# Kernel tuning notes

Hardware: AMD Instinct MI355X
Metric: run time of the kernel (lower is better)

Reference implementation:

```python
import jax, jax.numpy as jnp
import numpy as np

D_MODEL, N_HEADS, D_FF = 1024, 16, 4096
NUM_FAMILIES, DICT_SIZE = 64, 16384
B, T = 2, 2048
EPS = 1e-6


def setup_inputs() -> dict:
    key = jax.random.key(0)
    ks = jax.random.split(key, 16)
    s = 0.02
    return {
        "x": jax.random.normal(ks[0], (B, T, D_MODEL), jnp.float32),
        "top_k": 8,
        "proto": jax.random.normal(ks[1], (NUM_FAMILIES, D_MODEL), jnp.float32) * s,
        "family_gate_w": jax.random.normal(ks[2], (NUM_FAMILIES, D_MODEL), jnp.float32) * s,
        "dict_w": jax.random.normal(ks[3], (DICT_SIZE, D_MODEL), jnp.float32) * s,
        "enc_w": jax.random.normal(ks[4], (DICT_SIZE, D_MODEL), jnp.float32) * s,
        "wq": jax.random.normal(ks[5], (D_MODEL, D_MODEL), jnp.float32) * s,
        "wk": jax.random.normal(ks[6], (D_MODEL, D_MODEL), jnp.float32) * s,
        "wv": jax.random.normal(ks[7], (D_MODEL, D_MODEL), jnp.float32) * s,
        "wo": jax.random.normal(ks[8], (D_MODEL, D_MODEL), jnp.float32) * s,
        "rel_templates": jax.random.normal(ks[9], (N_HEADS, D_MODEL // N_HEADS, D_MODEL // N_HEADS), jnp.float32) * s,
        "gate_proj_w": jax.random.normal(ks[10], (D_FF, D_MODEL), jnp.float32) * s,
        "up_proj_w": jax.random.normal(ks[11], (D_FF, D_MODEL), jnp.float32) * s,
        "down_proj_w": jax.random.normal(ks[12], (D_MODEL, D_FF), jnp.float32) * s,
        "norm1_w": jnp.ones((D_MODEL,), jnp.float32),
        "norm2_w": jnp.ones((D_MODEL,), jnp.float32),
        "bias_corr": jnp.zeros((D_MODEL,), jnp.float32),
    }


def _hc_norm(x, w):
    rms = jnp.sqrt(jnp.mean(x * x, axis=-1, keepdims=True) + EPS)
    return w * x / rms, jnp.mean(rms)


def _block(x, top_k, proto, family_gate_w, dict_w, enc_w, wq, wk, wv, wo,
           rel_templates, gate_proj_w, up_proj_w, down_proj_w,
           norm1_w, norm2_w, bias_corr):
    b, t, d = x.shape
    h = rel_templates.shape[0]
    dh = d // h
    m = dict_w.shape[0]

    # FamilyBasisPool
    family_scores = jax.nn.softmax(x @ family_gate_w.T, axis=-1)   # [b,t,K]
    basis = jnp.einsum('btk,kd->btd', family_scores, proto)

    # SparseOffsetDict on residual
    resid = x - basis
    coeffs = resid @ enc_w.T                                        # [b,t,M]
    topk_vals, topk_idx = jax.lax.top_k(coeffs, top_k)              # [b,t,k]
    # sparse scatter + einsum == gather rows of dictionary and weight them
    offset = jnp.einsum('btk,btkd->btd', topk_vals, dict_w[topk_idx])
    sparsity = jnp.sum(jnp.abs(topk_vals)) / (b * t * m)

    x_rec = basis + offset + bias_corr
    normed, e1 = _hc_norm(x_rec, norm1_w)

    # RelationProtocolLayer (k modulated by per-head templates)
    q = (normed @ wq.T).reshape(b, t, h, dh).transpose(0, 2, 1, 3)  # [b,h,t,dh]
    k = (normed @ wk.T).reshape(b, t, h, dh).transpose(0, 2, 1, 3)
    v = (normed @ wv.T).reshape(b, t, h, dh).transpose(0, 2, 1, 3)
    k_mod = jnp.einsum('bhtd,hde->bhte', k, rel_templates)
    attn = jax.nn.softmax(jnp.einsum('bhqd,bhkd->bhqk', q, k_mod) / jnp.sqrt(jnp.float32(dh)), axis=-1)
    out = jnp.einsum('bhqk,bhkd->bhqd', attn, v)
    out = out.transpose(0, 2, 1, 3).reshape(b, t, d) @ wo.T
    x = x + out

    normed2, e2 = _hc_norm(x, norm2_w)

    # ContextGatedRouter (sigmoid gate * silu up)
    gate = jax.nn.sigmoid(normed2 @ gate_proj_w.T)
    up = jax.nn.silu(normed2 @ up_proj_w.T)
    routed = (gate * up) @ down_proj_w.T
    x = x + routed
    return x, attn, family_scores, sparsity, e1, e2


def reference(x, top_k, proto, family_gate_w, dict_w, enc_w, wq, wk, wv, wo,
              rel_templates, gate_proj_w, up_proj_w, down_proj_w,
              norm1_w, norm2_w, bias_corr):
    return _block(x, top_k, proto, family_gate_w, dict_w, enc_w, wq, wk, wv, wo,
                  rel_templates, gate_proj_w, up_proj_w, down_proj_w,
                  norm1_w, norm2_w, bias_corr)
```

## Files before the change

kernel.cpp:

```cpp
#include <hip/hip_runtime.h>
#include <float.h>
#include <math.h>

#define D 1024
#define NF 64
#define MDICT 16384
#define NH 16
#define DH 64
#define TT 2048
#define ROWS 4096
#define DFF 4096

#define OUT_X     0LL
#define OUT_ATTN  4194304LL
#define OUT_FS    138412032LL
#define OUT_SPARS 138674176LL
#define OUT_E1    138674177LL
#define OUT_E2    138674178LL

typedef __attribute__((ext_vector_type(8))) short short8;
typedef __attribute__((ext_vector_type(4))) float f32x4;

__device__ inline unsigned short f2bf(float f) {
    unsigned int u = __float_as_uint(f);
    u = u + 0x7FFFu + ((u >> 16) & 1u);
    return (unsigned short)(u >> 16);
}
__device__ inline float bf2f(unsigned int s) {
    return __uint_as_float(s << 16);
}

__device__ inline float blk_sum(float v) {
    __shared__ float sb[4];
    int lane = threadIdx.x & 63, w = threadIdx.x >> 6;
#pragma unroll
    for (int o = 32; o; o >>= 1) v += __shfl_down(v, o);
    if (lane == 0) sb[w] = v;
    __syncthreads();
    float s = sb[0] + sb[1] + sb[2] + sb[3];
    __syncthreads();
    return s;
}

template<int BM, int BN, bool OBF, bool ACONV>
__global__ __launch_bounds__(256) void gemm_mfma(
    const void* __restrict__ Abv, const unsigned short* __restrict__ Bb,
    void* __restrict__ Cbv, const float* __restrict__ addCb,
    int K, int lda, int ldb, int ldc, float alpha, int batchH,
    long long aOut, long long aIn, long long bOut, long long bIn,
    long long cOut, long long cIn)
{
    int z = blockIdx.z;
    int zo = z / batchH, zi = z - zo * batchH;
    long long aoff = zo * aOut + zi * aIn;
    const unsigned short* B = Bb + zo * bOut + zi * bIn;
    long long cbase = zo * cOut + zi * cIn;
    const float* addC = addCb ? (addCb + cbase) : nullptr;

    __shared__ __align__(16) unsigned short As[BM * 32];
    __shared__ __align__(16) unsigned short Bs[BN * 32];

    int tid = threadIdx.x;
    int lane = tid & 63, wave = tid >> 6;
    int wr = wave >> 1, wc = wave & 1;
    long long r0 = (long long)blockIdx.y * BM;
    long long c0 = (long long)blockIdx.x * BN;

    constexpr int TI = BM / 32;
    constexpr int TJ = BN / 32;
    constexpr int RA = BM * 4 / 256;
    constexpr int RB = BN * 4 / 256;

    f32x4 acc[TI][TJ] = {};
    int lm = lane & 15;
    int kq = (lane >> 4) * 8;

    for (int k0 = 0; k0 < K; k0 += 32) {
        __syncthreads();
#pragma unroll
        for (int r = 0; r < RB; r++) {
            int q = r * 256 + tid;
            const unsigned short* gp = B + (c0 + (q >> 2)) * (long long)ldb + k0 + (q & 3) * 8;
            unsigned short* lp = Bs + (r * 256 + (tid & 192)) * 8;
            __builtin_amdgcn_global_load_lds(
                (const __attribute__((address_space(1))) void*)gp,
                (__attribute__((address_space(3))) void*)lp, 16, 0, 0);
        }
        if (ACONV) {
            const float* A = (const float*)Abv + aoff;
#pragma unroll
            for (int r = 0; r < RA; r++) {
                int q = r * 256 + tid;
                const float* gp = A + (r0 + (q >> 2)) * (long long)lda + k0 + (q & 3) * 8;
                float4 v0 = *(const float4*)gp;
                float4 v1 = *(const float4*)(gp + 4);
                short8 f;
                f[0] = (short)f2bf(v0.x); f[1] = (short)f2bf(v0.y);
                f[2] = (short)f2bf(v0.z); f[3] = (short)f2bf(v0.w);
                f[4] = (short)f2bf(v1.x); f[5] = (short)f2bf(v1.y);
                f[6] = (short)f2bf(v1.z); f[7] = (short)f2bf(v1.w);
                *(short8*)&As[q * 8] = f;
            }
        } else {
            const unsigned short* A = (const unsigned short*)Abv + aoff;
#pragma unroll
            for (int r = 0; r < RA; r++) {
                int q = r * 256 + tid;
                const unsigned short* gp = A + (r0 + (q >> 2)) * (long long)lda + k0 + (q & 3) * 8;
                unsigned short* lp = As + (r * 256 + (tid & 192)) * 8;
                __builtin_amdgcn_global_load_lds(
                    (const __attribute__((address_space(1))) void*)gp,
                    (__attribute__((address_space(3))) void*)lp, 16, 0, 0);
            }
        }
        __syncthreads();
        short8 af[TI], bfr[TJ];
#pragma unroll
        for (int i = 0; i < TI; i++)
            af[i] = *(const short8*)&As[(wr * (BM / 2) + i * 16 + lm) * 32 + kq];
#pragma unroll
        for (int j = 0; j < TJ; j++)
            bfr[j] = *(const short8*)&Bs[(wc * (BN / 2) + j * 16 + lm) * 32 + kq];
#pragma unroll
        for (int i = 0; i < TI; i++)
#pragma unroll
            for (int j = 0; j < TJ; j++)
                acc[i][j] = __builtin_amdgcn_mfma_f32_16x16x32_bf16(af[i], bfr[j], acc[i][j], 0, 0, 0);
    }

#pragma unroll
    for (int i = 0; i < TI; i++) {
#pragma unroll
        for (int r = 0; r < 4; r++) {
            long long row = r0 + wr * (BM / 2) + i * 16 + (lane >> 4) * 4 + r;
#pragma unroll
            for (int j = 0; j < TJ; j++) {
                long long col = c0 + wc * (BN / 2) + j * 16 + lm;
                long long idx = row * (long long)ldc + col;
                float v = alpha * acc[i][j][r];
                if (addC) v += addC[idx];
                if (OBF) ((unsigned short*)Cbv)[cbase + idx] = f2bf(v);
                else     ((float*)Cbv)[cbase + idx] = v;
            }
        }
    }
}

__global__ __launch_bounds__(256) void cvt_bf16_kernel(
    const float* __restrict__ in, unsigned short* __restrict__ out, long long n4)
{
    long long i = (long long)blockIdx.x * 256 + threadIdx.x;
    long long stride = (long long)gridDim.x * 256;
    for (; i < n4; i += stride) {
        float4 v = ((const float4*)in)[i];
        uint2 p;
        p.x = (unsigned)f2bf(v.x) | ((unsigned)f2bf(v.y) << 16);
        p.y = (unsigned)f2bf(v.z) | ((unsigned)f2bf(v.w) << 16);
        ((uint2*)out)[i] = p;
    }
}

__global__ __launch_bounds__(64) void family_kernel(
    const float* __restrict__ x, const float* __restrict__ fgw,
    float* __restrict__ fs_out)
{
    __shared__ float xs[D];
    int r = blockIdx.x, f = threadIdx.x;
    const float4* x4 = (const float4*)(x + (long long)r * D);
    float4* xs4 = (float4*)xs;
#pragma unroll
    for (int i = 0; i < 4; i++) xs4[f + 64 * i] = x4[f + 64 * i];
    __syncthreads();
    const float4* w4 = (const float4*)(fgw + (long long)f * D);
    float acc = 0.f;
#pragma unroll 8
    for (int d = 0; d < D / 4; d++) {
        float4 w = w4[d];
        float4 xv = xs4[d];
        acc += w.x * xv.x + w.y * xv.y + w.z * xv.z + w.w * xv.w;
    }
    float mx = acc;
#pragma unroll
    for (int o = 32; o; o >>= 1) mx = fmaxf(mx, __shfl_xor(mx, o));
    float e = __expf(acc - mx);
    float s = e;
#pragma unroll
    for (int o = 32; o; o >>= 1) s += __shfl_xor(s, o);
    fs_out[(long long)r * NF + f] = e / s;
}

__global__ __launch_bounds__(256) void basis_kernel(
    const float* __restrict__ x, const float* __restrict__ fs,
    const float* __restrict__ proto, float* __restrict__ basis,
    unsigned short* __restrict__ resid_bf)
{
    __shared__ float Ss[NF];
    int r = blockIdx.x, tid = threadIdx.x;
    if (tid < NF) Ss[tid] = fs[(long long)r * NF + tid];
    __syncthreads();
    float4 acc = {0.f, 0.f, 0.f, 0.f};
    const float4* p4 = (const float4*)proto;
#pragma unroll 8
    for (int k = 0; k < NF; k++) {
        float s = Ss[k];
        float4 p = p4[k * (D / 4) + tid];
        acc.x += s * p.x; acc.y += s * p.y; acc.z += s * p.z; acc.w += s * p.w;
    }
    long long base = (long long)r * (D / 4) + tid;
    float4 xv = ((const float4*)x)[base];
    ((float4*)basis)[base] = acc;
    uint2 rp;
    rp.x = (unsigned)f2bf(xv.x - acc.x) | ((unsigned)f2bf(xv.y - acc.y) << 16);
    rp.y = (unsigned)f2bf(xv.z - acc.z) | ((unsigned)f2bf(xv.w - acc.w) << 16);
    ((uint2*)resid_bf)[base] = rp;
}

__device__ inline void ins8(float v, int idx, float* vs, int* is) {
    if (v <= vs[7]) return;
    vs[7] = v; is[7] = idx;
#pragma unroll
    for (int j = 7; j > 0; j--) {
        if (vs[j] > vs[j - 1]) {
            float tv = vs[j]; vs[j] = vs[j - 1]; vs[j - 1] = tv;
            int ti = is[j]; is[j] = is[j - 1]; is[j - 1] = ti;
        }
    }
}

__global__ __launch_bounds__(256) void topk_kernel(
    const float* __restrict__ coeffs, float* __restrict__ tkv,
    int* __restrict__ tki, float* __restrict__ spars_acc)
{
    __shared__ float sv[2624];
    __shared__ int   si[2624];
    int r = blockIdx.x, tid = threadIdx.x;
    const float* row = coeffs + (long long)r * MDICT;
    float vs[8]; int is[8];
#pragma unroll
    for (int j = 0; j < 8; j++) { vs[j] = -FLT_MAX; is[j] = -1; }
    for (int s = 0; s < MDICT / 256; s++) {
        int col = s * 256 + tid;
        ins8(row[col], col, vs, is);
    }
#pragma unroll
    for (int j = 0; j < 8; j++) { sv[tid * 8 + j] = vs[j]; si[tid * 8 + j] = is[j]; }
    __syncthreads();
    if (tid < 64) {
#pragma unroll
        for (int j = 0; j < 8; j++) { vs[j] = -FLT_MAX; is[j] = -1; }
        for (int e = tid * 32; e < tid * 32 + 32; e++) ins8(sv[e], si[e], vs, is);
#pragma unroll
        for (int j = 0; j < 8; j++) { sv[2048 + tid * 8 + j] = vs[j]; si[2048 + tid * 8 + j] = is[j]; }
    }
    __syncthreads();
    if (tid < 8) {
#pragma unroll
        for (int j = 0; j < 8; j++) { vs[j] = -FLT_MAX; is[j] = -1; }
        for (int e = 2048 + tid * 64; e < 2048 + tid * 64 + 64; e++) ins8(sv[e], si[e], vs, is);
#pragma unroll
        for (int j = 0; j < 8; j++) { sv[2560 + tid * 8 + j] = vs[j]; si[2560 + tid * 8 + j] = is[j]; }
    }
    __syncthreads();
    if (tid == 0) {
#pragma unroll
        for (int j = 0; j < 8; j++) { vs[j] = -FLT_MAX; is[j] = -1; }
        for (int e = 2560; e < 2624; e++) ins8(sv[e], si[e], vs, is);
        float s = 0.f;
#pragma unroll
        for (int j = 0; j < 8; j++) {
            tkv[r * 8 + j] = vs[j];
            tki[r * 8 + j] = is[j];
            s += fabsf(vs[j]);
        }
        atomicAdd(spars_acc, s);
    }
}

__global__ __launch_bounds__(256) void xrec_norm_kernel(
    const float* __restrict__ basis, const float* __restrict__ dictw,
    const float* __restrict__ bias, const float* __restrict__ nw,
    const float* __restrict__ tkv, const int* __restrict__ tki,
    unsigned short* __restrict__ normed_bf, float* __restrict__ e_acc)
{
    int r = blockIdx.x, tid = threadIdx.x;
    float vals[8]; int idxs[8];
#pragma unroll
    for (int j = 0; j < 8; j++) { vals[j] = tkv[r * 8 + j]; idxs[j] = tki[r * 8 + j]; }
    long long base = (long long)r * (D / 4) + tid;
    float4 acc = ((const float4*)basis)[base];
    float4 bv = ((const float4*)bias)[tid];
    acc.x += bv.x; acc.y += bv.y; acc.z += bv.z; acc.w += bv.w;
#pragma unroll
    for (int j = 0; j < 8; j++) {
        float4 dv = ((const float4*)dictw)[(long long)idxs[j] * (D / 4) + tid];
        float v = vals[j];
        acc.x += v * dv.x; acc.y += v * dv.y; acc.z += v * dv.z; acc.w += v * dv.w;
    }
    float ss = acc.x * acc.x + acc.y * acc.y + acc.z * acc.z + acc.w * acc.w;
    float tot = blk_sum(ss);
    float rms = sqrtf(tot / (float)D + 1e-6f);
    if (tid == 0) atomicAdd(e_acc, rms);
    float inv = 1.f / rms;
    float4 wv = ((const float4*)nw)[tid];
    uint2 o;
    o.x = (unsigned)f2bf(acc.x * wv.x * inv) | ((unsigned)f2bf(acc.y * wv.y * inv) << 16);
    o.y = (unsigned)f2bf(acc.z * wv.z * inv) | ((unsigned)f2bf(acc.w * wv.w * inv) << 16);
    ((uint2*)normed_bf)[base] = o;
}

__global__ __launch_bounds__(256) void rmsnorm_kernel(
    const float* __restrict__ xin, const float* __restrict__ nw,
    unsigned short* __restrict__ xout_bf, float* __restrict__ e_acc)
{
    int r = blockIdx.x, tid = threadIdx.x;
    long long base = (long long)r * (D / 4) + tid;
    float4 v = ((const float4*)xin)[base];
    float ss = v.x * v.x + v.y * v.y + v.z * v.z + v.w * v.w;
    float tot = blk_sum(ss);
    float rms = sqrtf(tot / (float)D + 1e-6f);
    if (tid == 0) atomicAdd(e_acc, rms);
    float inv = 1.f / rms;
    float4 wv = ((const float4*)nw)[tid];
    uint2 o;
    o.x = (unsigned)f2bf(v.x * wv.x * inv) | ((unsigned)f2bf(v.y * wv.y * inv) << 16);
    o.y = (unsigned)f2bf(v.z * wv.z * inv) | ((unsigned)f2bf(v.w * wv.w * inv) << 16);
    ((uint2*)xout_bf)[base] = o;
}

__global__ __launch_bounds__(256) void kmod_kernel(
    const unsigned short* __restrict__ kb, const float* __restrict__ rel,
    unsigned short* __restrict__ kmod_bf)
{
    __shared__ float Rs[64 * 64];
    int z = blockIdx.y;
    int b = z >> 4, h = z & 15;
    int tid = threadIdx.x;
    const float4* r4 = (const float4*)(rel + (long long)h * 4096);
    float4* Rs4 = (float4*)Rs;
#pragma unroll
    for (int i = 0; i < 4; i++) Rs4[tid + 256 * i] = r4[tid + 256 * i];
    __syncthreads();
    int e = tid & 63, tl = tid >> 6;
    int t = blockIdx.x * 4 + tl;
    const unsigned short* krow = kb + ((long long)(b * TT + t)) * D + h * DH;
    float acc = 0.f;
#pragma unroll
    for (int d4 = 0; d4 < 16; d4++) {
        uint2 p = *(const uint2*)&krow[d4 * 4];
        acc += bf2f(p.x & 0xFFFFu) * Rs[(d4 * 4 + 0) * 64 + e];
        acc += bf2f(p.x >> 16)     * Rs[(d4 * 4 + 1) * 64 + e];
        acc += bf2f(p.y & 0xFFFFu) * Rs[(d4 * 4 + 2) * 64 + e];
        acc += bf2f(p.y >> 16)     * Rs[(d4 * 4 + 3) * 64 + e];
    }
    kmod_bf[(long long)z * (TT * DH) + t * 64 + e] = f2bf(acc);
}

__global__ __launch_bounds__(256) void vtrans_kernel(
    const unsigned short* __restrict__ vb, unsigned short* __restrict__ vT)
{
    __shared__ unsigned short tile[64][68];
    int z = blockIdx.y, b = z >> 4, h = z & 15;
    int t0 = blockIdx.x * 64;
    int tid = threadIdx.x;
    int tr = tid >> 4;
    int dc = (tid & 15) * 4;
#pragma unroll
    for (int r = 0; r < 4; r++) {
        int t = tr + r * 16;
        uint2 p = *(const uint2*)&vb[((long long)(b * TT + t0 + t)) * D + h * DH + dc];
        tile[t][dc] = (unsigned short)(p.x & 0xFFFFu);
        tile[t][dc + 1] = (unsigned short)(p.x >> 16);
        tile[t][dc + 2] = (unsigned short)(p.y & 0xFFFFu);
        tile[t][dc + 3] = (unsigned short)(p.y >> 16);
    }
    __syncthreads();
#pragma unroll
    for (int r = 0; r < 4; r++) {
        int d = tr + r * 16;
        int t = (tid & 15) * 4;
        uint2 p;
        p.x = (unsigned)tile[t][d] | ((unsigned)tile[t + 1][d] << 16);
        p.y = (unsigned)tile[t + 2][d] | ((unsigned)tile[t + 3][d] << 16);
        *(uint2*)&vT[(long long)z * 64 * TT + (long long)d * TT + t0 + t] = p;
    }
}

__global__ __launch_bounds__(256, 2) void attn_fused_kernel(
    const unsigned short* __restrict__ qb,
    const unsigned short* __restrict__ kmod,
    const unsigned short* __restrict__ vT,
    float* __restrict__ attn,
    unsigned short* __restrict__ ctx)
{
    constexpr int QS_LD = 72;
    constexpr int PS_LD = 136;
    __shared__ __align__(16) unsigned short Qs[128 * QS_LD];
    __shared__ __align__(16) unsigned short Ks[128 * QS_LD];
    __shared__ __align__(16) unsigned short Ps[128 * PS_LD];
    __shared__ float sm_h[2][128];
    __shared__ float sl_h[2][128];

    const int z = blockIdx.y;
    const int b = z >> 4, h = z & 15;
    const int q0 = blockIdx.x * 128;
    const int tid = threadIdx.x;
    const int lane = tid & 63;
    const int wave = tid >> 6;
    const int wr = wave >> 1, wc = wave & 1;
    const int lm = lane & 15, q4 = lane >> 4;
    const int kq = q4 * 8;

    {
        const unsigned short* qbase = qb + ((long long)(b * TT + q0)) * D + h * DH;
#pragma unroll
        for (int rr = 0; rr < 4; rr++) {
            int q = rr * 256 + tid;
            int row = q >> 3, seg = q & 7;
            short8 v = *(const short8*)(qbase + (long long)row * D + seg * 8);
            *(short8*)&Qs[row * QS_LD + seg * 8] = v;
        }
    }

    const unsigned short* kz = kmod + (long long)z * (TT * DH);

    float m_loc[4][4], l_loc[4][4];
#pragma unroll
    for (int i = 0; i < 4; i++)
#pragma unroll
        for (int r = 0; r < 4; r++) { m_loc[i][r] = -FLT_MAX; l_loc[i][r] = 0.f; }

    for (int kt = 0; kt < 16; kt++) {
        __syncthreads();
#pragma unroll
        for (int rr = 0; rr < 4; rr++) {
            int q = rr * 256 + tid;
            int row = q >> 3, seg = q & 7;
            short8 v = *(const short8*)(kz + (long long)(kt * 128 + row) * DH + seg * 8);
            *(short8*)&Ks[row * QS_LD + seg * 8] = v;
        }
        __syncthreads();
        f32x4 acc[4][4] = {};
#pragma unroll
        for (int ks = 0; ks < 2; ks++) {
            short8 af[4], bfk[4];
#pragma unroll
            for (int i = 0; i < 4; i++)
                af[i] = *(const short8*)&Qs[(wr * 64 + i * 16 + lm) * QS_LD + ks * 32 + kq];
#pragma unroll
            for (int j = 0; j < 4; j++)
                bfk[j] = *(const short8*)&Ks[(wc * 64 + j * 16 + lm) * QS_LD + ks * 32 + kq];
#pragma unroll
            for (int i = 0; i < 4; i++)
#pragma unroll
                for (int j = 0; j < 4; j++)
                    acc[i][j] = __builtin_amdgcn_mfma_f32_16x16x32_bf16(af[i], bfk[j], acc[i][j], 0, 0, 0);
        }
#pragma unroll
        for (int i = 0; i < 4; i++)
#pragma unroll
            for (int r = 0; r < 4; r++) {
                float v0 = acc[i][0][r] * 0.125f;
                float v1 = acc[i][1][r] * 0.125f;
                float v2 = acc[i][2][r] * 0.125f;
                float v3 = acc[i][3][r] * 0.125f;
                float tmax = fmaxf(fmaxf(v0, v1), fmaxf(v2, v3));
                float mo = m_loc[i][r];
                float mn = fmaxf(mo, tmax);
                l_loc[i][r] = l_loc[i][r] * __expf(mo - mn)
                            + __expf(v0 - mn) + __expf(v1 - mn)
                            + __expf(v2 - mn) + __expf(v3 - mn);
                m_loc[i][r] = mn;
            }
    }

#pragma unroll
    for (int off = 1; off <= 8; off <<= 1) {
#pragma unroll
        for (int i = 0; i < 4; i++)
#pragma unroll
            for (int r = 0; r < 4; r++) {
                float mo = __shfl_xor(m_loc[i][r], off);
                float lo = __shfl_xor(l_loc[i][r], off);
                float mn = fmaxf(m_loc[i][r], mo);
                l_loc[i][r] = l_loc[i][r] * __expf(m_loc[i][r] - mn) + lo * __expf(mo - mn);
                m_loc[i][r] = mn;
            }
    }
    if (lm == 0) {
#pragma unroll
        for (int i = 0; i < 4; i++)
#pragma unroll
            for (int r = 0; r < 4; r++) {
                int row = wr * 64 + i * 16 + q4 * 4 + r;
                sm_h[wc][row] = m_loc[i][r];
                sl_h[wc][row] = l_loc[i][r];
            }
    }
    __syncthreads();
    float Mf[4][4], Linv[4][4];
#pragma unroll
    for (int i = 0; i < 4; i++)
#pragma unroll
        for (int r = 0; r < 4; r++) {
            int row = wr * 64 + i * 16 + q4 * 4 + r;
            float m0 = sm_h[0][row], m1 = sm_h[1][row];
            float l0 = sl_h[0][row], l1 = sl_h[1][row];
            float mn = fmaxf(m0, m1);
            float L = l0 * __expf(m0 - mn) + l1 * __expf(m1 - mn);
            Mf[i][r] = mn;
            Linv[i][r] = 1.f / L;
        }

    const unsigned short* vz = vT + (long long)z * (64 * TT);
    float* az = attn + (long long)z * ((long long)TT * TT);
    f32x4 acc_o[4][2] = {};

    for (int kt = 0; kt < 16; kt++) {
        __syncthreads();
#pragma unroll
        for (int rr = 0; rr < 4; rr++) {
            int q = rr * 256 + tid;
            int row = q >> 3, seg = q & 7;
            short8 v = *(const short8*)(kz + (long long)(kt * 128 + row) * DH + seg * 8);
            *(short8*)&Ks[row * QS_LD + seg * 8] = v;
        }
        short8 bv[2][4];
#pragma unroll
        for (int j = 0; j < 2; j++)
#pragma unroll
            for (int ks = 0; ks < 4; ks++)
                bv[j][ks] = *(const short8*)(vz + (long long)(wc * 32 + j * 16 + lm) * TT
                                             + kt * 128 + ks * 32 + kq);
        __syncthreads();
        f32x4 acc[4][4] = {};
#pragma unroll
        for (int ks = 0; ks < 2; ks++) {
            short8 af[4], bfk[4];
#pragma unroll
            for (int i = 0; i < 4; i++)
                af[i] = *(const short8*)&Qs[(wr * 64 + i * 16 + lm) * QS_LD + ks * 32 + kq];
#pragma unroll
            for (int j = 0; j < 4; j++)
                bfk[j] = *(const short8*)&Ks[(wc * 64 + j * 16 + lm) * QS_LD + ks * 32 + kq];
#pragma unroll
            for (int i = 0; i < 4; i++)
#pragma unroll
                for (int j = 0; j < 4; j++)
                    acc[i][j] = __builtin_amdgcn_mfma_f32_16x16x32_bf16(af[i], bfk[j], acc[i][j], 0, 0, 0);
        }
#pragma unroll
        for (int i = 0; i < 4; i++)
#pragma unroll
            for (int r = 0; r < 4; r++) {
                int row = wr * 64 + i * 16 + q4 * 4 + r;
                float* arow = az + (long long)(q0 + row) * TT + kt * 128 + wc * 64 + lm;
#pragma unroll
                for (int j = 0; j < 4; j++) {
                    float p = __expf(acc[i][j][r] * 0.125f - Mf[i][r]) * Linv[i][r];
                    arow[j * 16] = p;
                    Ps[row * PS_LD + wc * 64 + j * 16 + lm] = f2bf(p);
                }
            }
        __syncthreads();
#pragma unroll
        for (int ks = 0; ks < 4; ks++) {
            short8 paf[4];
#pragma unroll
            for (int i = 0; i < 4; i++)
                paf[i] = *(const short8*)&Ps[(wr * 64 + i * 16 + lm) * PS_LD + ks * 32 + kq];
#pragma unroll
            for (int i = 0; i < 4; i++)
#pragma unroll
                for (int j = 0; j < 2; j++)
                    acc_o[i][j] = __builtin_amdgcn_mfma_f32_16x16x32_bf16(paf[i], bv[j][ks], acc_o[i][j], 0, 0, 0);
        }
    }

#pragma unroll
    for (int i = 0; i < 4; i++)
#pragma unroll
        for (int r = 0; r < 4; r++) {
            int row = wr * 64 + i * 16 + q4 * 4 + r;
            long long crow = ((long long)(b * TT + q0 + row)) * D + h * DH;
#pragma unroll
            for (int j = 0; j < 2; j++)
                ctx[crow + wc * 32 + j * 16 + lm] = f2bf(acc_o[i][j][r]);
        }
}

__global__ __launch_bounds__(256) void gateup_kernel(
    unsigned short* __restrict__ g, const unsigned short* __restrict__ u, long long n4)
{
    long long i = (long long)blockIdx.x * 256 + threadIdx.x;
    long long stride = (long long)gridDim.x * 256;
    for (; i < n4; i += stride) {
        uint2 gp = ((uint2*)g)[i];
        uint2 up = ((const uint2*)u)[i];
        float gv[4] = { bf2f(gp.x & 0xFFFFu), bf2f(gp.x >> 16), bf2f(gp.y & 0xFFFFu), bf2f(gp.y >> 16) };
        float uv[4] = { bf2f(up.x & 0xFFFFu), bf2f(up.x >> 16), bf2f(up.y & 0xFFFFu), bf2f(up.y >> 16) };
        unsigned short hh[4];
#pragma unroll
        for (int j = 0; j < 4; j++) {
            float r = (1.f / (1.f + __expf(-gv[j]))) * uv[j] * (1.f / (1.f + __expf(-uv[j])));
            hh[j] = f2bf(r);
        }
        uint2 o;
        o.x = (unsigned)hh[0] | ((unsigned)hh[1] << 16);
        o.y = (unsigned)hh[2] | ((unsigned)hh[3] << 16);
        ((uint2*)g)[i] = o;
    }
}

__global__ void finalize_kernel(const float* __restrict__ scal, float* __restrict__ out)
{
    out[OUT_SPARS] = scal[0] / (float)((double)ROWS * (double)MDICT);
    out[OUT_E1] = scal[1] / (float)ROWS;
    out[OUT_E2] = scal[2] / (float)ROWS;
}

extern "C" void kernel_launch(void* const* d_in, const int* in_sizes, int n_in,
                              void* d_out, int out_size, void* d_ws, size_t ws_size,
                              hipStream_t stream) {
    const float* x     = (const float*)d_in[0];
    const float* proto = (const float*)d_in[2];
    const float* fgw   = (const float*)d_in[3];
    const float* dictw = (const float*)d_in[4];
    const float* encw  = (const float*)d_in[5];
    const float* wq    = (const float*)d_in[6];
    const float* wk    = (const float*)d_in[7];
    const float* wv    = (const float*)d_in[8];
    const float* wo    = (const float*)d_in[9];
    const float* rel   = (const float*)d_in[10];
    const float* gatew = (const float*)d_in[11];
    const float* upw   = (const float*)d_in[12];
    const float* downw = (const float*)d_in[13];
    const float* n1w   = (const float*)d_in[14];
    const float* n2w   = (const float*)d_in[15];
    const float* bias  = (const float*)d_in[16];
    float* out = (float*)d_out;
    float* ws  = (float*)d_ws;

    float*          basisf  = ws + 0;
    unsigned short* kb_bf   = (unsigned short*)(ws + 4194304);
    unsigned short* resid_bf= (unsigned short*)(ws + 6291456);
    unsigned short* norm_bf = (unsigned short*)(ws + 8388608);
    unsigned short* qb_bf   = (unsigned short*)(ws + 10485760);
    unsigned short* vb_bf   = (unsigned short*)(ws + 12582912);
    unsigned short* kmod_bf = (unsigned short*)(ws + 14680064);
    unsigned short* vT_bf   = (unsigned short*)(ws + 16777216);
    unsigned short* encw_bf = (unsigned short*)(ws + 18874368);
    unsigned short* up_bf   = (unsigned short*)(ws + 27262976);
    unsigned short* wq_bf   = (unsigned short*)(ws + 35651584);
    unsigned short* wk_bf   = (unsigned short*)(ws + 36175872);
    unsigned short* wv_bf   = (unsigned short*)(ws + 36700160);
    unsigned short* wo_bf   = (unsigned short*)(ws + 37224448);
    unsigned short* gatew_bf= (unsigned short*)(ws + 37748736);
    unsigned short* upw_bf  = (unsigned short*)(ws + 39845888);
    unsigned short* downw_bf= (unsigned short*)(ws + 41943040);
    float*          tkv     = ws + 44040192;
    int*            tki     = (int*)(ws + 44072960);
    float*          scal    = ws + 44105728;
    unsigned short* ctx_bf  = resid_bf;
    unsigned short* gate_bf = encw_bf;
    float*          xmid    = basisf;

    float* fs   = out + OUT_FS;
    float* attn = out + OUT_ATTN;
    float* coeffs = attn;

    hipMemsetAsync(scal, 0, 3 * sizeof(float), stream);

    cvt_bf16_kernel<<<2048, 256, 0, stream>>>(encw, encw_bf, (long long)MDICT * D / 4);
    cvt_bf16_kernel<<<256, 256, 0, stream>>>(wq, wq_bf, (long long)D * D / 4);
    cvt_bf16_kernel<<<256, 256, 0, stream>>>(wk, wk_bf, (long long)D * D / 4);
    cvt_bf16_kernel<<<256, 256, 0, stream>>>(wv, wv_bf, (long long)D * D / 4);
    cvt_bf16_kernel<<<256, 256, 0, stream>>>(wo, wo_bf, (long long)D * D / 4);
    cvt_bf16_kernel<<<1024, 256, 0, stream>>>(gatew, gatew_bf, (long long)DFF * D / 4);
    cvt_bf16_kernel<<<1024, 256, 0, stream>>>(upw, upw_bf, (long long)DFF * D / 4);
    cvt_bf16_kernel<<<1024, 256, 0, stream>>>(downw, downw_bf, (long long)D * DFF / 4);

    family_kernel<<<ROWS, 64, 0, stream>>>(x, fgw, fs);
    basis_kernel<<<ROWS, 256, 0, stream>>>(x, fs, proto, basisf, resid_bf);
    gemm_mfma<128, 128, false, false><<<dim3(128, 32, 1), 256, 0, stream>>>(
        resid_bf, encw_bf, coeffs, nullptr, D, D, D, MDICT, 1.f, 1, 0, 0, 0, 0, 0, 0);
    topk_kernel<<<ROWS, 256, 0, stream>>>(coeffs, tkv, tki, scal + 0);
    xrec_norm_kernel<<<ROWS, 256, 0, stream>>>(basisf, dictw, bias, n1w, tkv, tki, norm_bf, scal + 1);
    gemm_mfma<128, 128, true, false><<<dim3(8, 32, 1), 256, 0, stream>>>(
        norm_bf, wq_bf, qb_bf, nullptr, D, D, D, D, 1.f, 1, 0, 0, 0, 0, 0, 0);
    gemm_mfma<128, 128, true, false><<<dim3(8, 32, 1), 256, 0, stream>>>(
        norm_bf, wk_bf, kb_bf, nullptr, D, D, D, D, 1.f, 1, 0, 0, 0, 0, 0, 0);
    gemm_mfma<128, 128, true, false><<<dim3(8, 32, 1), 256, 0, stream>>>(
        norm_bf, wv_bf, vb_bf, nullptr, D, D, D, D, 1.f, 1, 0, 0, 0, 0, 0, 0);
    kmod_kernel<<<dim3(TT / 4, 32), 256, 0, stream>>>(kb_bf, rel, kmod_bf);
    vtrans_kernel<<<dim3(TT / 64, 32), 256, 0, stream>>>(vb_bf, vT_bf);
    attn_fused_kernel<<<dim3(TT / 128, 32), 256, 0, stream>>>(
        qb_bf, kmod_bf, vT_bf, attn, ctx_bf);
    gemm_mfma<128, 128, false, false><<<dim3(8, 32, 1), 256, 0, stream>>>(
        ctx_bf, wo_bf, xmid, x, D, D, D, D, 1.f, 1, 0, 0, 0, 0, 0, 0);
    rmsnorm_kernel<<<ROWS, 256, 0, stream>>>(xmid, n2w, norm_bf, scal + 2);
    gemm_mfma<128, 128, true, false><<<dim3(32, 32, 1), 256, 0, stream>>>(
        norm_bf, gatew_bf, gate_bf, nullptr, D, D, D, DFF, 1.f, 1, 0, 0, 0, 0, 0, 0);
    gemm_mfma<128, 128, true, false><<<dim3(32, 32, 1), 256, 0, stream>>>(
        norm_bf, upw_bf, up_bf, nullptr, D, D, D, DFF, 1.f, 1, 0, 0, 0, 0, 0, 0);
    gateup_kernel<<<4096, 256, 0, stream>>>(gate_bf, up_bf, (long long)ROWS * DFF / 4);
    gemm_mfma<128, 128, false, false><<<dim3(8, 32, 1), 256, 0, stream>>>(
        gate_bf, downw_bf, out + OUT_X, xmid, DFF, DFF, DFF, D, 1.f, 1, 0, 0, 0, 0, 0, 0);
    finalize_kernel<<<1, 1, 0, stream>>>(scal, out);
}
```

Baseline: 2.026 ms.

## Fuse top-k into encoder GEMM, merge QKV and gate/up GEMMs, add XCD swizzle

The encoder GEMM now computes per-tile top-8 candidates in its epilogue, so the full 4096x16384 fp32 coefficient matrix is no longer written and re-read. A small reduction kernel then merges the candidates per row. The Q/K/V and gate/up projections are merged into single wider GEMMs that rely on the weight buffers being contiguous. Downstream kernels index into the interleaved outputs, and workgroups are swizzled across XCDs for cache locality. The fused epilogue adds shared-memory pressure and serial insertion work to the GEMM.

```diff
diff --git a/kernel.cpp b/kernel.cpp
--- a/kernel.cpp
+++ b/kernel.cpp
@@ -10,6 +10,7 @@
 #define TT 2048
 #define ROWS 4096
 #define DFF 4096
+#define QKV_LD 3072
 
 #define OUT_X     0LL
 #define OUT_ATTN  4194304LL
@@ -30,6 +31,12 @@
     return __uint_as_float(s << 16);
 }
 
+__device__ inline int xcd_swz(int wg, int nwg) {
+    int q = nwg >> 3, r = nwg & 7;
+    int xcd = wg & 7, loc = wg >> 3;
+    return (xcd < r ? xcd * (q + 1) : r * (q + 1) + (xcd - r) * q) + loc;
+}
+
 __device__ inline float blk_sum(float v) {
     __shared__ float sb[4];
     int lane = threadIdx.x & 63, w = threadIdx.x >> 6;
@@ -42,20 +49,19 @@
     return s;
 }
 
-template<int BM, int BN, bool OBF, bool ACONV>
+template<int BM, int BN, bool OBF>
 __global__ __launch_bounds__(256) void gemm_mfma(
-    const void* __restrict__ Abv, const unsigned short* __restrict__ Bb,
+    const unsigned short* __restrict__ Ab, const unsigned short* __restrict__ Bb,
     void* __restrict__ Cbv, const float* __restrict__ addCb,
-    int K, int lda, int ldb, int ldc, float alpha, int batchH,
-    long long aOut, long long aIn, long long bOut, long long bIn,
-    long long cOut, long long cIn)
-{
-    int z = blockIdx.z;
-    int zo = z / batchH, zi = z - zo * batchH;
-    long long aoff = zo * aOut + zi * aIn;
-    const unsigned short* B = Bb + zo * bOut + zi * bIn;
-    long long cbase = zo * cOut + zi * cIn;
-    const float* addC = addCb ? (addCb + cbase) : nullptr;
+    int K, int lda, int ldb, int ldc, float alpha)
+{
+    int nwg = gridDim.x * gridDim.y;
+    int wg = blockIdx.y * gridDim.x + blockIdx.x;
+    int swz = xcd_swz(wg, nwg);
+    int bx = swz % (int)gridDim.x, by = swz / (int)gridDim.x;
+
+    const unsigned short* B = Bb;
+    const float* addC = addCb;
 
     __shared__ __align__(16) unsigned short As[BM * 32];
     __shared__ __align__(16) unsigned short Bs[BN * 32];
@@ -63,8 +69,8 @@
     int tid = threadIdx.x;
     int lane = tid & 63, wave = tid >> 6;
     int wr = wave >> 1, wc = wave & 1;
-    long long r0 = (long long)blockIdx.y * BM;
-    long long c0 = (long long)blockIdx.x * BN;
+    long long r0 = (long long)by * BM;
+    long long c0 = (long long)bx * BN;
 
     constexpr int TI = BM / 32;
     constexpr int TJ = BN / 32;
@@ -86,32 +92,14 @@
                 (const __attribute__((address_space(1))) void*)gp,
                 (__attribute__((address_space(3))) void*)lp, 16, 0, 0);
         }
-        if (ACONV) {
-            const float* A = (const float*)Abv + aoff;
-#pragma unroll
-            for (int r = 0; r < RA; r++) {
-                int q = r * 256 + tid;
-                const float* gp = A + (r0 + (q >> 2)) * (long long)lda + k0 + (q & 3) * 8;
-                float4 v0 = *(const float4*)gp;
-                float4 v1 = *(const float4*)(gp + 4);
-                short8 f;
-                f[0] = (short)f2bf(v0.x); f[1] = (short)f2bf(v0.y);
-                f[2] = (short)f2bf(v0.z); f[3] = (short)f2bf(v0.w);
-                f[4] = (short)f2bf(v1.x); f[5] = (short)f2bf(v1.y);
-                f[6] = (short)f2bf(v1.z); f[7] = (short)f2bf(v1.w);
-                *(short8*)&As[q * 8] = f;
-            }
-        } else {
-            const unsigned short* A = (const unsigned short*)Abv + aoff;
-#pragma unroll
-            for (int r = 0; r < RA; r++) {
-                int q = r * 256 + tid;
-                const unsigned short* gp = A + (r0 + (q >> 2)) * (long long)lda + k0 + (q & 3) * 8;
-                unsigned short* lp = As + (r * 256 + (tid & 192)) * 8;
-                __builtin_amdgcn_global_load_lds(
-                    (const __attribute__((address_space(1))) void*)gp,
-                    (__attribute__((address_space(3))) void*)lp, 16, 0, 0);
-            }
+#pragma unroll
+        for (int r = 0; r < RA; r++) {
+            int q = r * 256 + tid;
+            const unsigned short* gp = Ab + (r0 + (q >> 2)) * (long long)lda + k0 + (q & 3) * 8;
+            unsigned short* lp = As + (r * 256 + (tid & 192)) * 8;
+            __builtin_amdgcn_global_load_lds(
+                (const __attribute__((address_space(1))) void*)gp,
+                (__attribute__((address_space(3))) void*)lp, 16, 0, 0);
         }
         __syncthreads();
         short8 af[TI], bfr[TJ];
@@ -139,10 +127,170 @@
                 long long idx = row * (long long)ldc + col;
                 float v = alpha * acc[i][j][r];
                 if (addC) v += addC[idx];
-                if (OBF) ((unsigned short*)Cbv)[cbase + idx] = f2bf(v);
-                else     ((float*)Cbv)[cbase + idx] = v;
+                if (OBF) ((unsigned short*)Cbv)[idx] = f2bf(v);
+                else     ((float*)Cbv)[idx] = v;
             }
         }
+    }
+}
+
+__device__ inline void ins8(float v, int idx, float* vs, int* is) {
+    if (v <= vs[7]) return;
+    vs[7] = v; is[7] = idx;
+#pragma unroll
+    for (int j = 7; j > 0; j--) {
+        if (vs[j] > vs[j - 1]) {
+            float tv = vs[j]; vs[j] = vs[j - 1]; vs[j - 1] = tv;
+            int ti = is[j]; is[j] = is[j - 1]; is[j - 1] = ti;
+        }
+    }
+}
+
+__global__ __launch_bounds__(256) void gemm_topk(
+    const unsigned short* __restrict__ Ab, const unsigned short* __restrict__ Bb,
+    float* __restrict__ cand_v, int* __restrict__ cand_i)
+{
+    constexpr int BM = 128, BN = 128;
+    constexpr int NBX = MDICT / BN;
+    int nwg = gridDim.x * gridDim.y;
+    int wg = blockIdx.y * gridDim.x + blockIdx.x;
+    int swz = xcd_swz(wg, nwg);
+    int bx = swz % (int)gridDim.x, by = swz / (int)gridDim.x;
+
+    __shared__ __align__(16) unsigned short As[BM * 32];
+    __shared__ __align__(16) unsigned short Bs[BN * 32];
+    __shared__ float Sv[64 * 133];
+
+    int tid = threadIdx.x;
+    int lane = tid & 63, wave = tid >> 6;
+    int wr = wave >> 1, wc = wave & 1;
+    long long r0 = (long long)by * BM;
+    long long c0 = (long long)bx * BN;
+
+    f32x4 acc[4][4] = {};
+    int lm = lane & 15;
+    int q4 = lane >> 4;
+    int kq = q4 * 8;
+
+    for (int k0 = 0; k0 < D; k0 += 32) {
+        __syncthreads();
+#pragma unroll
+        for (int r = 0; r < 2; r++) {
+            int q = r * 256 + tid;
+            const unsigned short* gp = Bb + (c0 + (q >> 2)) * (long long)D + k0 + (q & 3) * 8;
+            unsigned short* lp = Bs + (r * 256 + (tid & 192)) * 8;
+            __builtin_amdgcn_global_load_lds(
+                (const __attribute__((address_space(1))) void*)gp,
+                (__attribute__((address_space(3))) void*)lp, 16, 0, 0);
+        }
+#pragma unroll
+        for (int r = 0; r < 2; r++) {
+            int q = r * 256 + tid;
+            const unsigned short* gp = Ab + (r0 + (q >> 2)) * (long long)D + k0 + (q & 3) * 8;
+            unsigned short* lp = As + (r * 256 + (tid & 192)) * 8;
+            __builtin_amdgcn_global_load_lds(
+                (const __attribute__((address_space(1))) void*)gp,
+                (__attribute__((address_space(3))) void*)lp, 16, 0, 0);
+        }
+        __syncthreads();
+        short8 af[4], bfr[4];
+#pragma unroll
+        for (int i = 0; i < 4; i++)
+            af[i] = *(const short8*)&As[(wr * 64 + i * 16 + lm) * 32 + kq];
+#pragma unroll
+        for (int j = 0; j < 4; j++)
+            bfr[j] = *(const short8*)&Bs[(wc * 64 + j * 16 + lm) * 32 + kq];
+#pragma unroll
+        for (int i = 0; i < 4; i++)
+#pragma unroll
+            for (int j = 0; j < 4; j++)
+                acc[i][j] = __builtin_amdgcn_mfma_f32_16x16x32_bf16(af[i], bfr[j], acc[i][j], 0, 0, 0);
+    }
+
+#pragma unroll
+    for (int h = 0; h < 2; h++) {
+        __syncthreads();
+        if (wr == h) {
+#pragma unroll
+            for (int i = 0; i < 4; i++)
+#pragma unroll
+                for (int r = 0; r < 4; r++)
+#pragma unroll
+                    for (int j = 0; j < 4; j++)
+                        Sv[(i * 16 + q4 * 4 + r) * 133 + wc * 64 + j * 16 + lm] = acc[i][j][r];
+        }
+        __syncthreads();
+        int row_loc = tid >> 2, sub = tid & 3;
+        float vs[8]; int is[8];
+#pragma unroll
+        for (int k = 0; k < 8; k++) { vs[k] = -FLT_MAX; is[k] = -1; }
+        const float* Srow = &Sv[row_loc * 133 + sub * 32];
+        int cbase = (int)c0 + sub * 32;
+        for (int c = 0; c < 32; c++) ins8(Srow[c], cbase + c, vs, is);
+#pragma unroll
+        for (int step = 1; step <= 2; step <<= 1) {
+            float ov[8]; int oi[8];
+#pragma unroll
+            for (int k = 0; k < 8; k++) { ov[k] = __shfl_xor(vs[k], step); oi[k] = __shfl_xor(is[k], step); }
+#pragma unroll
+            for (int k = 0; k < 8; k++) ins8(ov[k], oi[k], vs, is);
+        }
+        if (sub == 0) {
+            long long grow = r0 + h * 64 + row_loc;
+#pragma unroll
+            for (int k = 0; k < 8; k++) {
+                cand_v[grow * (NBX * 8) + bx * 8 + k] = vs[k];
+                cand_i[grow * (NBX * 8) + bx * 8 + k] = is[k];
+            }
+        }
+    }
+}
+
+__global__ __launch_bounds__(256) void topk_reduce_kernel(
+    const float* __restrict__ cand_v, const int* __restrict__ cand_i,
+    float* __restrict__ tkv, int* __restrict__ tki, float* __restrict__ spars_acc)
+{
+    __shared__ float sv[2624];
+    __shared__ int   si[2624];
+    int r = blockIdx.x, tid = threadIdx.x;
+    float4 cv = ((const float4*)(cand_v + (long long)r * 1024))[tid];
+    int4   ci = ((const int4*)(cand_i + (long long)r * 1024))[tid];
+    float vs[8]; int is[8];
+#pragma unroll
+    for (int j = 0; j < 8; j++) { vs[j] = -FLT_MAX; is[j] = -1; }
+    ins8(cv.x, ci.x, vs, is); ins8(cv.y, ci.y, vs, is);
+    ins8(cv.z, ci.z, vs, is); ins8(cv.w, ci.w, vs, is);
+#pragma unroll
+    for (int j = 0; j < 8; j++) { sv[tid * 8 + j] = vs[j]; si[tid * 8 + j] = is[j]; }
+    __syncthreads();
+    if (tid < 64) {
+#pragma unroll
+        for (int j = 0; j < 8; j++) { vs[j] = -FLT_MAX; is[j] = -1; }
+        for (int e = tid * 32; e < tid * 32 + 32; e++) ins8(sv[e], si[e], vs, is);
+#pragma unroll
+        for (int j = 0; j < 8; j++) { sv[2048 + tid * 8 + j] = vs[j]; si[2048 + tid * 8 + j] = is[j]; }
+    }
+    __syncthreads();
+    if (tid < 8) {
+#pragma unroll
+        for (int j = 0; j < 8; j++) { vs[j] = -FLT_MAX; is[j] = -1; }
+        for (int e = 2048 + tid * 64; e < 2048 + tid * 64 + 64; e++) ins8(sv[e], si[e], vs, is);
+#pragma unroll
+        for (int j = 0; j < 8; j++) { sv[2560 + tid * 8 + j] = vs[j]; si[2560 + tid * 8 + j] = is[j]; }
+    }
+    __syncthreads();
+    if (tid == 0) {
+#pragma unroll
+        for (int j = 0; j < 8; j++) { vs[j] = -FLT_MAX; is[j] = -1; }
+        for (int e = 2560; e < 2624; e++) ins8(sv[e], si[e], vs, is);
+        float s = 0.f;
+#pragma unroll
+        for (int j = 0; j < 8; j++) {
+            tkv[r * 8 + j] = vs[j];
+            tki[r * 8 + j] = is[j];
+            s += fabsf(vs[j]);
+        }
+        atomicAdd(spars_acc, s);
     }
 }
 
@@ -213,67 +361,6 @@
     rp.x = (unsigned)f2bf(xv.x - acc.x) | ((unsigned)f2bf(xv.y - acc.y) << 16);
     rp.y = (unsigned)f2bf(xv.z - acc.z) | ((unsigned)f2bf(xv.w - acc.w) << 16);
     ((uint2*)resid_bf)[base] = rp;
-}
-
-__device__ inline void ins8(float v, int idx, float* vs, int* is) {
-    if (v <= vs[7]) return;
-    vs[7] = v; is[7] = idx;
-#pragma unroll
-    for (int j = 7; j > 0; j--) {
-        if (vs[j] > vs[j - 1]) {
-            float tv = vs[j]; vs[j] = vs[j - 1]; vs[j - 1] = tv;
-            int ti = is[j]; is[j] = is[j - 1]; is[j - 1] = ti;
-        }
-    }
-}
-
-__global__ __launch_bounds__(256) void topk_kernel(
-    const float* __restrict__ coeffs, float* __restrict__ tkv,
-    int* __restrict__ tki, float* __restrict__ spars_acc)
-{
-    __shared__ float sv[2624];
-    __shared__ int   si[2624];
-    int r = blockIdx.x, tid = threadIdx.x;
-    const float* row = coeffs + (long long)r * MDICT;
-    float vs[8]; int is[8];
-#pragma unroll
-    for (int j = 0; j < 8; j++) { vs[j] = -FLT_MAX; is[j] = -1; }
-    for (int s = 0; s < MDICT / 256; s++) {
-        int col = s * 256 + tid;
-        ins8(row[col], col, vs, is);
-    }
-#pragma unroll
-    for (int j = 0; j < 8; j++) { sv[tid * 8 + j] = vs[j]; si[tid * 8 + j] = is[j]; }
-    __syncthreads();
-    if (tid < 64) {
-#pragma unroll
-        for (int j = 0; j < 8; j++) { vs[j] = -FLT_MAX; is[j] = -1; }
-        for (int e = tid * 32; e < tid * 32 + 32; e++) ins8(sv[e], si[e], vs, is);
-#pragma unroll
-        for (int j = 0; j < 8; j++) { sv[2048 + tid * 8 + j] = vs[j]; si[2048 + tid * 8 + j] = is[j]; }
-    }
-    __syncthreads();
-    if (tid < 8) {
-#pragma unroll
-        for (int j = 0; j < 8; j++) { vs[j] = -FLT_MAX; is[j] = -1; }
-        for (int e = 2048 + tid * 64; e < 2048 + tid * 64 + 64; e++) ins8(sv[e], si[e], vs, is);
-#pragma unroll
-        for (int j = 0; j < 8; j++) { sv[2560 + tid * 8 + j] = vs[j]; si[2560 + tid * 8 + j] = is[j]; }
-    }
-    __syncthreads();
-    if (tid == 0) {
-#pragma unroll
-        for (int j = 0; j < 8; j++) { vs[j] = -FLT_MAX; is[j] = -1; }
-        for (int e = 2560; e < 2624; e++) ins8(sv[e], si[e], vs, is);
-        float s = 0.f;
-#pragma unroll
-        for (int j = 0; j < 8; j++) {
-            tkv[r * 8 + j] = vs[j];
-            tki[r * 8 + j] = is[j];
-            s += fabsf(vs[j]);
-        }
-        atomicAdd(spars_acc, s);
-    }
 }
 
 __global__ __launch_bounds__(256) void xrec_norm_kernel(
@@ -328,7 +415,7 @@
 }
 
 __global__ __launch_bounds__(256) void kmod_kernel(
-    const unsigned short* __restrict__ kb, const float* __restrict__ rel,
+    const unsigned short* __restrict__ qkv, const float* __restrict__ rel,
     unsigned short* __restrict__ kmod_bf)
 {
     __shared__ float Rs[64 * 64];
@@ -342,7 +429,7 @@
     __syncthreads();
     int e = tid & 63, tl = tid >> 6;
     int t = blockIdx.x * 4 + tl;
-    const unsigned short* krow = kb + ((long long)(b * TT + t)) * D + h * DH;
+    const unsigned short* krow = qkv + ((long long)(b * TT + t)) * QKV_LD + D + h * DH;
     float acc = 0.f;
 #pragma unroll
     for (int d4 = 0; d4 < 16; d4++) {
@@ -356,7 +443,7 @@
 }
 
 __global__ __launch_bounds__(256) void vtrans_kernel(
-    const unsigned short* __restrict__ vb, unsigned short* __restrict__ vT)
+    const unsigned short* __restrict__ qkv, unsigned short* __restrict__ vT)
 {
     __shared__ unsigned short tile[64][68];
     int z = blockIdx.y, b = z >> 4, h = z & 15;
@@ -367,7 +454,7 @@
 #pragma unroll
     for (int r = 0; r < 4; r++) {
         int t = tr + r * 16;
-        uint2 p = *(const uint2*)&vb[((long long)(b * TT + t0 + t)) * D + h * DH + dc];
+        uint2 p = *(const uint2*)&qkv[((long long)(b * TT + t0 + t)) * QKV_LD + 2 * D + h * DH + dc];
         tile[t][dc] = (unsigned short)(p.x & 0xFFFFu);
         tile[t][dc + 1] = (unsigned short)(p.x >> 16);
         tile[t][dc + 2] = (unsigned short)(p.y & 0xFFFFu);
@@ -386,7 +473,7 @@
 }
 
 __global__ __launch_bounds__(256, 2) void attn_fused_kernel(
-    const unsigned short* __restrict__ qb,
+    const unsigned short* __restrict__ qkv,
     const unsigned short* __restrict__ kmod,
     const unsigned short* __restrict__ vT,
     float* __restrict__ attn,
@@ -400,9 +487,12 @@
     __shared__ float sm_h[2][128];
     __shared__ float sl_h[2][128];
 
-    const int z = blockIdx.y;
+    int nwg = gridDim.x * gridDim.y;
+    int wg = blockIdx.y * gridDim.x + blockIdx.x;
+    int swz = xcd_swz(wg, nwg);
+    const int z = swz / (int)gridDim.x;
+    const int q0 = (swz % (int)gridDim.x) * 128;
     const int b = z >> 4, h = z & 15;
-    const int q0 = blockIdx.x * 128;
     const int tid = threadIdx.x;
     const int lane = tid & 63;
     const int wave = tid >> 6;
@@ -411,12 +501,12 @@
     const int kq = q4 * 8;
 
     {
-        const unsigned short* qbase = qb + ((long long)(b * TT + q0)) * D + h * DH;
+        const unsigned short* qbase = qkv + ((long long)(b * TT + q0)) * QKV_LD + h * DH;
 #pragma unroll
         for (int rr = 0; rr < 4; rr++) {
             int q = rr * 256 + tid;
             int row = q >> 3, seg = q & 7;
-            short8 v = *(const short8*)(qbase + (long long)row * D + seg * 8);
+            short8 v = *(const short8*)(qbase + (long long)row * QKV_LD + seg * 8);
             *(short8*)&Qs[row * QS_LD + seg * 8] = v;
         }
     }
@@ -589,15 +679,19 @@
 }
 
 __global__ __launch_bounds__(256) void gateup_kernel(
-    unsigned short* __restrict__ g, const unsigned short* __restrict__ u, long long n4)
+    unsigned short* __restrict__ gu, long long n4)
 {
     long long i = (long long)blockIdx.x * 256 + threadIdx.x;
     long long stride = (long long)gridDim.x * 256;
+    uint2* gu2 = (uint2*)gu;
     for (; i < n4; i += stride) {
-        uint2 gp = ((uint2*)g)[i];
-        uint2 up = ((const uint2*)u)[i];
-        float gv[4] = { bf2f(gp.x & 0xFFFFu), bf2f(gp.x >> 16), bf2f(gp.y & 0xFFFFu), bf2f(gp.y >> 16) };
-        float uv[4] = { bf2f(up.x & 0xFFFFu), bf2f(up.x >> 16), bf2f(up.y & 0xFFFFu), bf2f(up.y >> 16) };
+        long long row = i >> 10, c = i & 1023;
+        uint2* gp = gu2 + row * 2048 + c;
+        const uint2* up = gu2 + row * 2048 + 1024 + c;
+        uint2 g = *gp;
+        uint2 u = *up;
+        float gv[4] = { bf2f(g.x & 0xFFFFu), bf2f(g.x >> 16), bf2f(g.y & 0xFFFFu), bf2f(g.y >> 16) };
+        float uv[4] = { bf2f(u.x & 0xFFFFu), bf2f(u.x >> 16), bf2f(u.y & 0xFFFFu), bf2f(u.y >> 16) };
         unsigned short hh[4];
 #pragma unroll
         for (int j = 0; j < 4; j++) {
@@ -607,7 +701,7 @@
         uint2 o;
         o.x = (unsigned)hh[0] | ((unsigned)hh[1] << 16);
         o.y = (unsigned)hh[2] | ((unsigned)hh[3] << 16);
-        ((uint2*)g)[i] = o;
+        *gp = o;
     }
 }
 
@@ -641,15 +735,13 @@
     float* ws  = (float*)d_ws;
 
     float*          basisf  = ws + 0;
-    unsigned short* kb_bf   = (unsigned short*)(ws + 4194304);
-    unsigned short* resid_bf= (unsigned short*)(ws + 6291456);
-    unsigned short* norm_bf = (unsigned short*)(ws + 8388608);
-    unsigned short* qb_bf   = (unsigned short*)(ws + 10485760);
-    unsigned short* vb_bf   = (unsigned short*)(ws + 12582912);
-    unsigned short* kmod_bf = (unsigned short*)(ws + 14680064);
-    unsigned short* vT_bf   = (unsigned short*)(ws + 16777216);
+    unsigned short* qkv_bf  = (unsigned short*)(ws + 4194304);
+    unsigned short* kmod_bf = (unsigned short*)(ws + 10485760);
+    unsigned short* vT_bf   = (unsigned short*)(ws + 12582912);
+    unsigned short* resid_bf= (unsigned short*)(ws + 14680064);
+    unsigned short* norm_bf = (unsigned short*)(ws + 16777216);
     unsigned short* encw_bf = (unsigned short*)(ws + 18874368);
-    unsigned short* up_bf   = (unsigned short*)(ws + 27262976);
+    unsigned short* gu_bf   = (unsigned short*)(ws + 18874368);
     unsigned short* wq_bf   = (unsigned short*)(ws + 35651584);
     unsigned short* wk_bf   = (unsigned short*)(ws + 36175872);
     unsigned short* wv_bf   = (unsigned short*)(ws + 36700160);
@@ -661,12 +753,12 @@
     int*            tki     = (int*)(ws + 44072960);
     float*          scal    = ws + 44105728;
     unsigned short* ctx_bf  = resid_bf;
-    unsigned short* gate_bf = encw_bf;
     float*          xmid    = basisf;
 
     float* fs   = out + OUT_FS;
     float* attn = out + OUT_ATTN;
-    float* coeffs = attn;
+    float* cand_v = attn;
+    int*   cand_i = (int*)(attn + 4194304);
 
     hipMemsetAsync(scal, 0, 3 * sizeof(float), stream);
 
@@ -681,29 +773,22 @@
 
     family_kernel<<<ROWS, 64, 0, stream>>>(x, fgw, fs);
     basis_kernel<<<ROWS, 256, 0, stream>>>(x, fs, proto, basisf, resid_bf);
-    gemm_mfma<128, 128, false, false><<<dim3(128, 32, 1), 256, 0, stream>>>(
-        resid_bf, encw_bf, coeffs, nullptr, D, D, D, MDICT, 1.f, 1, 0, 0, 0, 0, 0, 0);
-    topk_kernel<<<ROWS, 256, 0, stream>>>(coeffs, tkv, tki, scal + 0);
+    gemm_topk<<<dim3(128, 32, 1), 256, 0, stream>>>(resid_bf, encw_bf, cand_v, cand_i);
+    topk_reduce_kernel<<<ROWS, 256, 0, stream>>>(cand_v, cand_i, tkv, tki, scal + 0);
     xrec_norm_kernel<<<ROWS, 256, 0, stream>>>(basisf, dictw, bias, n1w, tkv, tki, norm_bf, scal + 1);
-    gemm_mfma<128, 128, true, false><<<dim3(8, 32, 1), 256, 0, stream>>>(
-        norm_bf, wq_bf, qb_bf, nullptr, D, D, D, D, 1.f, 1, 0, 0, 0, 0, 0, 0);
-    gemm_mfma<128, 128, true, false><<<dim3(8, 32, 1), 256, 0, stream>>>(
-        norm_bf, wk_bf, kb_bf, nullptr, D, D, D, D, 1.f, 1, 0, 0, 0, 0, 0, 0);
-    gemm_mfma<128, 128, true, false><<<dim3(8, 32, 1), 256, 0, stream>>>(
-        norm_bf, wv_bf, vb_bf, nullptr, D, D, D, D, 1.f, 1, 0, 0, 0, 0, 0, 0);
-    kmod_kernel<<<dim3(TT / 4, 32), 256, 0, stream>>>(kb_bf, rel, kmod_bf);
-    vtrans_kernel<<<dim3(TT / 64, 32), 256, 0, stream>>>(vb_bf, vT_bf);
+    gemm_mfma<128, 128, true><<<dim3(24, 32, 1), 256, 0, stream>>>(
+        norm_bf, wq_bf, qkv_bf, nullptr, D, D, D, QKV_LD, 1.f);
+    kmod_kernel<<<dim3(TT / 4, 32), 256, 0, stream>>>(qkv_bf, rel, kmod_bf);
+    vtrans_kernel<<<dim3(TT / 64, 32), 256, 0, stream>>>(qkv_bf, vT_bf);
     attn_fused_kernel<<<dim3(TT / 128, 32), 256, 0, stream>>>(
-        qb_bf, kmod_bf, vT_bf, attn, ctx_bf);
-    gemm_mfma<128, 128, false, false><<<dim3(8, 32, 1), 256, 0, stream>>>(
-        ctx_bf, wo_bf, xmid, x, D, D, D, D, 1.f, 1, 0, 0, 0, 0, 0, 0);
+        qkv_bf, kmod_bf, vT_bf, attn, ctx_bf);
+    gemm_mfma<128, 128, false><<<dim3(8, 32, 1), 256, 0, stream>>>(
+        ctx_bf, wo_bf, xmid, x, D, D, D, D, 1.f);
     rmsnorm_kernel<<<ROWS, 256, 0, stream>>>(xmid, n2w, norm_bf, scal + 2);
-    gemm_mfma<128, 128, true, false><<<dim3(32, 32, 1), 256, 0, stream>>>(
-        norm_bf, gatew_bf, gate_bf, nullptr, D, D, D, DFF, 1.f, 1, 0, 0, 0, 0, 0, 0);
-    gemm_mfma<128, 128, true, false><<<dim3(32, 32, 1), 256, 0, stream>>>(
-        norm_bf, upw_bf, up_bf, nullptr, D, D, D, DFF, 1.f, 1, 0, 0, 0, 0, 0, 0);
-    gateup_kernel<<<4096, 256, 0, stream>>>(gate_bf, up_bf, (long long)ROWS * DFF / 4);
-    gemm_mfma<128, 128, false, false><<<dim3(8, 32, 1), 256, 0, stream>>>(
-        gate_bf, downw_bf, out + OUT_X, xmid, DFF, DFF, DFF, D, 1.f, 1, 0, 0, 0, 0, 0, 0);
+    gemm_mfma<128, 128, true><<<dim3(64, 32, 1), 256, 0, stream>>>(
+        norm_bf, gatew_bf, gu_bf, nullptr, D, D, D, 2 * DFF, 1.f);
+    gateup_kernel<<<4096, 256, 0, stream>>>(gu_bf, (long long)ROWS * DFF / 4);
+    gemm_mfma<128, 128, false><<<dim3(8, 32, 1), 256, 0, stream>>>(
+        gu_bf, downw_bf, out + OUT_X, xmid, DFF, 2 * DFF, DFF, D, 1.f);
     finalize_kernel<<<1, 1, 0, stream>>>(scal, out);
 }
```

Result: faster. 1.944 ms (-4.1%).
